# Optimization experiments

Hardware: AMD Instinct MI355X
Metric: run time of the kernel (lower is better)

The kernel has to match this reference:

```python
import jax, jax.numpy as jnp
import numpy as np

V, E, H2, B, T, OUT = 50000, 300, 512, 32, 512, 256
H = H2 // 2  # hidden per direction


def _rand_mask(key, lengths, n_true):
    # exactly n_true True positions per row, all within the valid prefix [0, len)
    t = jnp.arange(T)[None, :]
    r = jax.random.uniform(key, (B, T)) + (t >= lengths[:, None]) * 10.0
    idx = jnp.argsort(r, axis=1)[:, :n_true]
    mask = jnp.zeros((B, T), dtype=bool)
    return mask.at[jnp.arange(B)[:, None], idx].set(True)


def setup_inputs() -> dict:
    key = jax.random.key(0)
    ks = jax.random.split(key, 12)
    inputs = jax.random.randint(ks[0], (B, T), 0, V)
    lengths = jnp.sort(jax.random.randint(ks[1], (B,), OUT, T + 1))[::-1]
    lengths = lengths.at[0].set(T)  # max length == padded length
    fmask = _rand_mask(ks[2], lengths, OUT)
    bmask = _rand_mask(ks[3], lengths, OUT)
    emb_scale = np.sqrt(3.0 / E).astype(np.float32)
    emb = jax.random.uniform(ks[4], (V, E), minval=-emb_scale, maxval=emb_scale, dtype=jnp.float32)
    k = 1.0 / np.sqrt(H).astype(np.float32)
    def u(kk, shape):
        return jax.random.uniform(kk, shape, minval=-k, maxval=k, dtype=jnp.float32)
    return {
        'inputs': inputs, 'seq_length': lengths, 'fmask': fmask, 'bmask': bmask,
        'out_seq_length': OUT, 'emb': emb,
        'W_ih_f': u(ks[5], (4 * H, E)), 'W_hh_f': u(ks[6], (4 * H, H)),
        'b_ih_f': u(ks[7], (4 * H,)), 'b_hh_f': u(ks[8], (4 * H,)),
        'W_ih_b': u(ks[9], (4 * H, E)), 'W_hh_b': u(ks[10], (4 * H, H)),
        'b_ih_b': u(ks[11], (4 * H,)), 'b_hh_b': u(ks[7], (4 * H,)),
    }


def run_lstm(xe, W_ih, W_hh, b_ih, b_hh):
    # PyTorch LSTM cell, gate order i,f,g,o. xe: (B,T,E) -> (B,T,H)
    xg = jnp.einsum('bte,ge->btg', xe, W_ih) + (b_ih + b_hh)
    def step(carry, xg_t):
        h, c = carry
        g = xg_t + h @ W_hh.T
        i, f, gg, o = jnp.split(g, 4, axis=-1)
        c = jax.nn.sigmoid(f) * c + jax.nn.sigmoid(i) * jnp.tanh(gg)
        h = jax.nn.sigmoid(o) * jnp.tanh(c)
        return (h, c), h
    h0 = jnp.zeros((xe.shape[0], W_hh.shape[1]), xe.dtype)
    _, hs = jax.lax.scan(step, (h0, h0), xg.transpose(1, 0, 2))
    return hs.transpose(1, 0, 2)


def select_masked(x, mask, out_len):
    # masked_select row-major order == indices of True in increasing t
    idx = jnp.argsort(jnp.logical_not(mask), axis=1, stable=True)[:, :out_len]
    return jnp.take_along_axis(x, idx[:, :, None], axis=1)


def reference(inputs, seq_length, fmask, bmask, out_seq_length, emb,
              W_ih_f, W_hh_f, b_ih_f, b_hh_f, W_ih_b, W_hh_b, b_ih_b, b_hh_b):
    t = jnp.arange(inputs.shape[1])[None, :]          # (1,T)
    valid = t < seq_length[:, None]                   # (B,T)
    # forward direction (dropout is identity at inference)
    f_out = run_lstm(emb[inputs], W_ih_f, W_hh_f, b_ih_f, b_hh_f)
    f_out = f_out * valid[..., None]                  # pad_packed zeros beyond len
    fsel = select_masked(f_out, fmask, out_seq_length)
    # per-batch sequence reversal of valid prefix (padding stays in place)
    rev_idx = jnp.where(valid, seq_length[:, None] - 1 - t, t)
    rinputs = jnp.take_along_axis(inputs, rev_idx, axis=1)
    b_out = run_lstm(emb[rinputs], W_ih_b, W_hh_b, b_ih_b, b_hh_b)
    b_out = b_out * valid[..., None]
    bsel = select_masked(b_out, bmask, out_seq_length)
    # re-reverse selected backward outputs per batch
    k = jnp.minimum(seq_length, out_seq_length)[:, None]
    t2 = jnp.arange(out_seq_length)[None, :]
    idx2 = jnp.where(t2 < k, out_seq_length - 1 - t2, t2 - k)
    bsel = jnp.take_along_axis(bsel, idx2[:, :, None], axis=1)
    return jnp.concatenate([fsel, bsel], axis=2)      # (B,out_seq,2H)
```

## Files before the change

### kernel.cpp

```cpp
#include <hip/hip_runtime.h>
#include <hip/hip_bf16.h>

#define B_   32
#define T_   512
#define E_   300
#define H_   256
#define OUT_ 256
#define ECH  100
#define GROWP 293

typedef unsigned long long u64;

__global__ __launch_bounds__(64) void slots_kernel(
    const unsigned char* __restrict__ fm, const unsigned char* __restrict__ bm,
    int* __restrict__ fslot, int* __restrict__ bpos)
{
    __shared__ unsigned char fL[B_ * T_];
    __shared__ unsigned char bL[B_ * T_];
    const int tid = threadIdx.x;

    const unsigned int* fw = (const unsigned int*)fm;
    int cnt = 0;
    for (int i = tid; i < 128; i += 64) {
        unsigned int v = fw[i];
        cnt += ((v & 0xFFu) != 0) + ((v & 0xFF00u) != 0)
             + ((v & 0xFF0000u) != 0) + ((v >> 24) != 0);
    }
#pragma unroll
    for (int off = 32; off; off >>= 1) cnt += __shfl_down(cnt, off, 64);
    bool isbool = __shfl(cnt, 0, 64) > 128;

    if (isbool) {
        for (int i = tid; i < B_ * T_ / 4; i += 64) {
            ((unsigned int*)fL)[i] = ((const unsigned int*)fm)[i];
            ((unsigned int*)bL)[i] = ((const unsigned int*)bm)[i];
        }
    } else {
        const unsigned int* bw = (const unsigned int*)bm;
        for (int i = tid; i < B_ * T_; i += 64) {
            fL[i] = fw[i] != 0;
            bL[i] = bw[i] != 0;
        }
    }
    __syncthreads();

    if (tid < B_) {
        int jf = 0, jb = 0;
        for (int t = 0; t < T_; ++t) {
            bool f = fL[tid * T_ + t] != 0;
            bool g = bL[tid * T_ + t] != 0;
            fslot[tid * T_ + t] = f ? (jf++) : -1;
            bpos [tid * T_ + t] = g ? (OUT_ - 1 - (jb++)) : -1;
        }
    }
}

__global__ __launch_bounds__(256) void xg_gemm(
    const int* __restrict__ inputs, const int* __restrict__ seqlen,
    const float* __restrict__ emb,
    const float* __restrict__ Wihf, const float* __restrict__ Wihb,
    const float* __restrict__ bihf, const float* __restrict__ bhhf,
    const float* __restrict__ bihb, const float* __restrict__ bhhb,
    float* __restrict__ xg, int t0, int TcMax)
{
    const int tg   = blockIdx.y;
    const int dir  = blockIdx.z;
    const int rblk = blockIdx.x * 64;
    const int tid  = threadIdx.x;

    __shared__ float eL[4][B_][ECH];
    __shared__ int   tokS[4][B_];

    if (tid < 128) {
        int t4 = tid >> 5, b = tid & 31;
        int t = t0 + tg * 4 + t4;
        int L = seqlen[b];
        int tt = t;
        if (dir) tt = (t < L) ? (L - 1 - t) : t;
        tokS[t4][b] = inputs[b * T_ + tt];
    }

    const float* W = dir ? Wihb : Wihf;
    const int b  = tid & 31;
    const int r8 = tid >> 5;

    float acc[4][8];
#pragma unroll
    for (int t4 = 0; t4 < 4; ++t4)
#pragma unroll
        for (int m = 0; m < 8; ++m) acc[t4][m] = 0.f;

    for (int ec = 0; ec < 3; ++ec) {
        __syncthreads();
        for (int idx = tid; idx < 3200; idx += 256) {
            int q  = idx % 25;
            int bb = (idx / 25) & 31;
            int t4 = idx / (25 * 32);
            const float* erow = emb + (size_t)tokS[t4][bb] * E_ + ec * ECH;
            *(float4*)&eL[t4][bb][q * 4] = *(const float4*)(erow + q * 4);
        }
        __syncthreads();

        for (int e4 = 0; e4 < 25; ++e4) {
            float4 w4[8];
#pragma unroll
            for (int m = 0; m < 8; ++m)
                w4[m] = *(const float4*)(W + (size_t)(rblk + r8 + m * 8) * E_
                                         + ec * ECH + e4 * 4);
#pragma unroll
            for (int t4 = 0; t4 < 4; ++t4) {
                float4 h4 = *(const float4*)&eL[t4][b][e4 * 4];
#pragma unroll
                for (int m = 0; m < 8; ++m)
                    acc[t4][m] += h4.x * w4[m].x + h4.y * w4[m].y
                                + h4.z * w4[m].z + h4.w * w4[m].w;
            }
        }
    }

    const float* bi = dir ? bihb : bihf;
    const float* bh = dir ? bhhb : bhhf;
#pragma unroll
    for (int t4 = 0; t4 < 4; ++t4) {
        float* outp = xg + (size_t)(dir * TcMax + tg * 4 + t4) * (1024 * B_);
#pragma unroll
        for (int m = 0; m < 8; ++m) {
            int row = rblk + r8 + m * 8;
            outp[(size_t)row * B_ + b] = acc[t4][m] + bi[row] + bh[row];
        }
    }
}

__global__ __launch_bounds__(512, 2) void fused_lstm(
    const int* __restrict__ inputs, const int* __restrict__ seqlen,
    const float* __restrict__ emb,
    const float* __restrict__ Wihf, const float* __restrict__ Whhf,
    const float* __restrict__ bihf, const float* __restrict__ bhhf,
    const float* __restrict__ Wihb, const float* __restrict__ Whhb,
    const float* __restrict__ bihb, const float* __restrict__ bhhb,
    const int* __restrict__ fslot, const int* __restrict__ bpos,
    float* __restrict__ hbuf, float* __restrict__ cbuf,
    int* __restrict__ barr, int* __restrict__ xgcnt,
    float* __restrict__ xg, float* __restrict__ out,
    int t0, int Tc, int fused)
{
    const int wg  = blockIdx.x;
    const int tid = threadIdx.x;
    __shared__ __align__(16) float smem[13824];

    if (wg >= 128) {
        float* eL   = smem;
        int*   tokS = (int*)(smem + 12800);
        const int hw = wg - 128;

        for (int j = hw; j < 2048; j += 128) {
            const int tg  = j >> 4;
            const int dir = (j >> 3) & 1;
            const int rp  = j & 7;
            const int rblk = (rp * 2 + (tid >> 8)) * 64;

            if (tid < 128) {
                int t4 = tid >> 5, b = tid & 31;
                int t = tg * 4 + t4;
                int L = seqlen[b];
                int tt = t;
                if (dir) tt = (t < L) ? (L - 1 - t) : t;
                tokS[t4 * B_ + b] = inputs[b * T_ + tt];
            }

            const float* W  = dir ? Wihb : Wihf;
            const int ltid = tid & 255;
            const int b  = ltid & 31;
            const int r8 = ltid >> 5;

            float acc[4][8];
#pragma unroll
            for (int t4 = 0; t4 < 4; ++t4)
#pragma unroll
                for (int m = 0; m < 8; ++m) acc[t4][m] = 0.f;

            for (int ec = 0; ec < 3; ++ec) {
                __syncthreads();
                for (int idx = tid; idx < 3200; idx += 512) {
                    int q  = idx % 25;
                    int bb = (idx / 25) & 31;
                    int t4 = idx / (25 * 32);
                    const float* erow = emb + (size_t)tokS[t4 * B_ + bb] * E_ + ec * ECH;
                    *(float4*)&eL[(t4 * B_ + bb) * ECH + q * 4] = *(const float4*)(erow + q * 4);
                }
                __syncthreads();

                for (int e4 = 0; e4 < 25; ++e4) {
                    float4 w4[8];
#pragma unroll
                    for (int m = 0; m < 8; ++m)
                        w4[m] = *(const float4*)(W + (size_t)(rblk + r8 + m * 8) * E_
                                                 + ec * ECH + e4 * 4);
#pragma unroll
                    for (int t4 = 0; t4 < 4; ++t4) {
                        float4 h4 = *(const float4*)&eL[(t4 * B_ + b) * ECH + e4 * 4];
#pragma unroll
                        for (int m = 0; m < 8; ++m)
                            acc[t4][m] += h4.x * w4[m].x + h4.y * w4[m].y
                                        + h4.z * w4[m].z + h4.w * w4[m].w;
                    }
                }
            }

            const float* bi = dir ? bihb : bihf;
            const float* bh = dir ? bhhb : bhhf;
#pragma unroll
            for (int t4 = 0; t4 < 4; ++t4) {
                float* outp = xg + (size_t)(dir * 512 + tg * 4 + t4) * (1024 * B_);
#pragma unroll
                for (int m = 0; m < 8; ++m) {
                    int row = rblk + r8 + m * 8;
                    __hip_atomic_store(&outp[(size_t)row * B_ + b],
                                       acc[t4][m] + bi[row] + bh[row],
                                       __ATOMIC_RELAXED, __HIP_MEMORY_SCOPE_AGENT);
                }
            }
            __syncthreads();
            if (tid == 0)
                __hip_atomic_fetch_add(&xgcnt[dir * 128 + tg], 1,
                                       __ATOMIC_RELAXED, __HIP_MEMORY_SCOPE_AGENT);
        }
        return;
    }

    float* hP   = smem;
    float* gbuf = smem + 8704;
    int*   sL   = (int*)(smem + 8704 + 4688);

    const int dir = wg >> 6;
    const int wgd = wg & 63;
    const int u0  = wgd * 4;

    const int rg  = tid & 3;
    const int bgr = (tid >> 2) & 7;
    const int kq  = tid >> 5;
    const int wv  = tid >> 6;
    const int lane = tid & 63;

    const float* Whh = dir ? Whhb : Whhf;

    float w[4][16];
#pragma unroll
    for (int r = 0; r < 4; ++r) {
        const float* wr = Whh + (size_t)(rg * H_ + u0 + r) * H_ + kq * 16;
#pragma unroll
        for (int q = 0; q < 4; ++q) {
            float4 v = *(const float4*)(wr + q * 4);
            w[r][q * 4 + 0] = v.x; w[r][q * 4 + 1] = v.y;
            w[r][q * 4 + 2] = v.z; w[r][q * 4 + 3] = v.w;
        }
    }
    if (tid < B_) sL[tid] = seqlen[tid];
    __syncthreads();

    const int ul = (tid >> 5) & 3, bb = tid & 31;
    float c_reg = 0.f;
    if (t0 > 0 && tid < 128)
        c_reg = cbuf[(size_t)(dir * 64 + wgd) * 128 + ul * 32 + bb];

    if (fused) {
        if (tid == 0) {
            const int* xc = xgcnt + dir * 128 + (t0 >> 2);
            while (__hip_atomic_load(xc, __ATOMIC_RELAXED,
                                     __HIP_MEMORY_SCOPE_AGENT) < 8)
                __builtin_amdgcn_s_sleep(1);
        }
        __syncthreads();
    }
    float xgv0 = 0.f, xgv1 = 0.f, xgv2 = 0.f, xgv3 = 0.f;
    if (tid < 128) {
        const float* xp = xg + (size_t)(dir * Tc) * 32768 + (u0 + ul) * 32 + bb;
        xgv0 = __hip_atomic_load(xp, __ATOMIC_RELAXED, __HIP_MEMORY_SCOPE_AGENT);
        xgv1 = __hip_atomic_load(xp + 256 * 32, __ATOMIC_RELAXED, __HIP_MEMORY_SCOPE_AGENT);
        xgv2 = __hip_atomic_load(xp + 512 * 32, __ATOMIC_RELAXED, __HIP_MEMORY_SCOPE_AGENT);
        xgv3 = __hip_atomic_load(xp + 768 * 32, __ATOMIC_RELAXED, __HIP_MEMORY_SCOPE_AGENT);
    }

    int* myflag = barr + dir * 64 + wgd;

    for (int tc = 0; tc < Tc; ++tc) {
        const int t = t0 + tc;

        if (tc > 0) {
            const int* fp = barr + dir * 64 + wv + 8 * (lane & 7);
            const int gneed = (fused && wv < 2 && tc + 1 < Tc) ? ((t0 + tc + 1) >> 2) : -1;
            const int* xc = xgcnt + dir * 128 + (gneed < 0 ? 0 : gneed);
            for (;;) {
                bool ok = __hip_atomic_load(fp, __ATOMIC_RELAXED,
                                            __HIP_MEMORY_SCOPE_AGENT) >= tc;
                if (gneed >= 0)
                    ok = ok && (__hip_atomic_load(xc, __ATOMIC_RELAXED,
                                                  __HIP_MEMORY_SCOPE_AGENT) >= 8);
                if (__all(ok)) break;
                __builtin_amdgcn_s_sleep(1);
            }
        }

        float xgn0 = 0.f, xgn1 = 0.f, xgn2 = 0.f, xgn3 = 0.f;
        if (tc + 1 < Tc && tid < 128) {
            const float* xp = xg + (size_t)(dir * Tc + tc + 1) * 32768 + (u0 + ul) * 32 + bb;
            xgn0 = __hip_atomic_load(xp, __ATOMIC_RELAXED, __HIP_MEMORY_SCOPE_AGENT);
            xgn1 = __hip_atomic_load(xp + 256 * 32, __ATOMIC_RELAXED, __HIP_MEMORY_SCOPE_AGENT);
            xgn2 = __hip_atomic_load(xp + 512 * 32, __ATOMIC_RELAXED, __HIP_MEMORY_SCOPE_AGENT);
            xgn3 = __hip_atomic_load(xp + 768 * 32, __ATOMIC_RELAXED, __HIP_MEMORY_SCOPE_AGENT);
        }

        if (t > 0) {
            const u64* hp64 = (const u64*)(hbuf +
                (size_t)(dir * 2 + ((t - 1) & 1)) * 8192);
            u64 hr[8];
#pragma unroll
            for (int i = 0; i < 8; ++i)
                hr[i] = __hip_atomic_load(hp64 + tid + 512 * i, __ATOMIC_RELAXED,
                                          __HIP_MEMORY_SCOPE_AGENT);
#pragma unroll
            for (int i = 0; i < 8; ++i) {
                int j = tid + 512 * i;
                int k  = (j >> 6) * 4 + ((j >> 4) & 3);
                int b0 = (j & 15) * 2;
                int addr = ((k >> 4) * 8 + (b0 >> 2)) * 68 + (k & 15) * 4 + (b0 & 3);
                *(u64*)&hP[addr] = hr[i];
            }
        }
        __syncthreads();

        float acc[4][4];
#pragma unroll
        for (int r = 0; r < 4; ++r)
#pragma unroll
            for (int bi = 0; bi < 4; ++bi) acc[r][bi] = 0.f;

        if (t > 0) {
            const float* hblk = &hP[(kq * 8 + bgr) * 68];
#pragma unroll
            for (int kk = 0; kk < 16; ++kk) {
                float4 h4 = *(const float4*)(hblk + kk * 4);
#pragma unroll
                for (int r = 0; r < 4; ++r) {
                    acc[r][0] += w[r][kk] * h4.x;
                    acc[r][1] += w[r][kk] * h4.y;
                    acc[r][2] += w[r][kk] * h4.z;
                    acc[r][3] += w[r][kk] * h4.w;
                }
            }
        }

#pragma unroll
        for (int r = 0; r < 4; ++r)
#pragma unroll
            for (int bi = 0; bi < 4; ++bi)
                acc[r][bi] += __shfl_xor(acc[r][bi], 32, 64);

        if (((tid >> 5) & 1) == 0) {
            const int kq2 = kq >> 1;
#pragma unroll
            for (int r = 0; r < 4; ++r)
#pragma unroll
                for (int bi = 0; bi < 4; ++bi)
                    gbuf[(r * 4 + rg) * GROWP + (bgr * 4 + bi) * 9 + kq2] = acc[r][bi];
        }
        __syncthreads();

        float hnew = 0.f;
        float* oaddr = nullptr;
        if (tid < 128) {
            const int u = u0 + ul;
            if (t < sL[bb]) {
                float gi = xgv0, gf = xgv1, gg = xgv2, go = xgv3;
#pragma unroll
                for (int q = 0; q < 8; ++q) {
                    gi += gbuf[(ul * 4 + 0) * GROWP + bb * 9 + q];
                    gf += gbuf[(ul * 4 + 1) * GROWP + bb * 9 + q];
                    gg += gbuf[(ul * 4 + 2) * GROWP + bb * 9 + q];
                    go += gbuf[(ul * 4 + 3) * GROWP + bb * 9 + q];
                }
                float si = 1.f / (1.f + expf(-gi));
                float sf = 1.f / (1.f + expf(-gf));
                float so = 1.f / (1.f + expf(-go));
                c_reg = sf * c_reg + si * tanhf(gg);
                hnew  = so * tanhf(c_reg);
                if (dir == 0) {
                    int j = fslot[bb * T_ + t];
                    if (j >= 0) oaddr = &out[((size_t)bb * OUT_ + j) * 512 + u];
                } else {
                    int p = bpos[bb * T_ + t];
                    if (p >= 0) oaddr = &out[((size_t)bb * OUT_ + p) * 512 + 256 + u];
                }
            } else {
                hnew = hP[((u >> 4) * 8 + (bb >> 2)) * 68 + (u & 15) * 4 + (bb & 3)];
            }
            float* hn = hbuf + (size_t)(dir * 2 + (t & 1)) * 8192;
            __hip_atomic_store(&hn[wgd * 128 + tid], hnew,
                               __ATOMIC_RELAXED, __HIP_MEMORY_SCOPE_AGENT);
        }
        xgv0 = xgn0; xgv1 = xgn1; xgv2 = xgn2; xgv3 = xgn3;
        __syncthreads();

        if (tc + 1 < Tc && tid == 0)
            __hip_atomic_store(myflag, tc + 1, __ATOMIC_RELAXED,
                               __HIP_MEMORY_SCOPE_AGENT);
        if (oaddr)
            __hip_atomic_store(oaddr, hnew, __ATOMIC_RELAXED,
                               __HIP_MEMORY_SCOPE_AGENT);
    }

    if (tid < 128)
        cbuf[(size_t)(dir * 64 + wgd) * 128 + ul * 32 + bb] = c_reg;
}

extern "C" void kernel_launch(void* const* d_in, const int* in_sizes, int n_in,
                              void* d_out, int out_size, void* d_ws, size_t ws_size,
                              hipStream_t stream) {
    const int*           inputs = (const int*)d_in[0];
    const int*           seqlen = (const int*)d_in[1];
    const unsigned char* fm     = (const unsigned char*)d_in[2];
    const unsigned char* bm     = (const unsigned char*)d_in[3];
    const float* emb  = (const float*)d_in[5];
    const float* Wihf = (const float*)d_in[6];
    const float* Whhf = (const float*)d_in[7];
    const float* bihf = (const float*)d_in[8];
    const float* bhhf = (const float*)d_in[9];
    const float* Wihb = (const float*)d_in[10];
    const float* Whhb = (const float*)d_in[11];
    const float* bihb = (const float*)d_in[12];
    const float* bhhb = (const float*)d_in[13];
    float* out = (float*)d_out;

    char* ws = (char*)d_ws;
    int*   fslot = (int*)(ws);
    int*   bpos  = (int*)(ws + 65536);
    float* hbuf  = (float*)(ws + 131072);
    float* cbuf  = (float*)(ws + 262144);
    int*   barr  = (int*)(ws + 327680);
    int*   xgcnt = (int*)(ws + 328192);
    float* xg    = (float*)(ws + 393216);
    (void)in_sizes; (void)n_in; (void)out_size;

    size_t avail = (ws_size > 393216) ? ws_size - 393216 : 0;
    int Tc = 4;
    for (int c = 512; c >= 4; c >>= 1)
        if ((size_t)c * 262144 <= avail) { Tc = c; break; }

    slots_kernel<<<1, 64, 0, stream>>>(fm, bm, fslot, bpos);

    if (Tc == 512) {
        (void)hipMemsetAsync(barr, 0, 512 + 1024, stream);
        fused_lstm<<<256, 512, 0, stream>>>(
            inputs, seqlen, emb, Wihf, Whhf, bihf, bhhf,
            Wihb, Whhb, bihb, bhhb, fslot, bpos,
            hbuf, cbuf, barr, xgcnt, xg, out, 0, 512, 1);
    } else {
        for (int t0 = 0; t0 < T_; t0 += Tc) {
            dim3 g(16, Tc / 4, 2);
            xg_gemm<<<g, 256, 0, stream>>>(inputs, seqlen, emb, Wihf, Wihb,
                                           bihf, bhhf, bihb, bhhb, xg, t0, Tc);
            (void)hipMemsetAsync(barr, 0, 512 + 1024, stream);
            fused_lstm<<<128, 512, 0, stream>>>(
                inputs, seqlen, emb, Wihf, Whhf, bihf, bhhf,
                Wihb, Whhb, bihb, bhhb, fslot, bpos,
                hbuf, cbuf, barr, xgcnt, xg, out, t0, Tc, 0);
        }
    }
}
```

Measured before the change: 2.039 ms.

## Replace flag barrier with step-tagged hidden-state packets and deepen xg prefetch

Each hidden value is now written as a 64-bit packet that carries the timestep alongside the float, so consumer workgroups spin directly on the h data instead of polling per-workgroup flags and then loading h separately. This removes one round trip through global memory and the separate flag store from every recurrent step. The input-gate prefetch now runs two steps ahead, and the wait on the xg producer counter moves off the critical path. In exchange the h traffic doubles in size, each poll reads 16 u64 values per thread, and hbuf must be zeroed up front.

```diff
diff --git a/kernel.cpp b/kernel.cpp
--- a/kernel.cpp
+++ b/kernel.cpp
@@ -139,9 +139,8 @@
     const float* __restrict__ Wihb, const float* __restrict__ Whhb,
     const float* __restrict__ bihb, const float* __restrict__ bhhb,
     const int* __restrict__ fslot, const int* __restrict__ bpos,
-    float* __restrict__ hbuf, float* __restrict__ cbuf,
-    int* __restrict__ barr, int* __restrict__ xgcnt,
-    float* __restrict__ xg, float* __restrict__ out,
+    u64* __restrict__ hbuf, float* __restrict__ cbuf,
+    int* __restrict__ xgcnt, float* __restrict__ xg, float* __restrict__ out,
     int t0, int Tc, int fused)
 {
     const int wg  = blockIdx.x;
@@ -239,8 +238,6 @@
     const int rg  = tid & 3;
     const int bgr = (tid >> 2) & 7;
     const int kq  = tid >> 5;
-    const int wv  = tid >> 6;
-    const int lane = tid & 63;
 
     const float* Whh = dir ? Whhb : Whhf;
 
@@ -272,62 +269,56 @@
         }
         __syncthreads();
     }
-    float xgv0 = 0.f, xgv1 = 0.f, xgv2 = 0.f, xgv3 = 0.f;
+    float xv0 = 0.f, xv1 = 0.f, xv2 = 0.f, xv3 = 0.f;
+    float ya0 = 0.f, ya1 = 0.f, ya2 = 0.f, ya3 = 0.f;
     if (tid < 128) {
         const float* xp = xg + (size_t)(dir * Tc) * 32768 + (u0 + ul) * 32 + bb;
-        xgv0 = __hip_atomic_load(xp, __ATOMIC_RELAXED, __HIP_MEMORY_SCOPE_AGENT);
-        xgv1 = __hip_atomic_load(xp + 256 * 32, __ATOMIC_RELAXED, __HIP_MEMORY_SCOPE_AGENT);
-        xgv2 = __hip_atomic_load(xp + 512 * 32, __ATOMIC_RELAXED, __HIP_MEMORY_SCOPE_AGENT);
-        xgv3 = __hip_atomic_load(xp + 768 * 32, __ATOMIC_RELAXED, __HIP_MEMORY_SCOPE_AGENT);
-    }
-
-    int* myflag = barr + dir * 64 + wgd;
+        xv0 = __hip_atomic_load(xp,         __ATOMIC_RELAXED, __HIP_MEMORY_SCOPE_AGENT);
+        xv1 = __hip_atomic_load(xp +  8192, __ATOMIC_RELAXED, __HIP_MEMORY_SCOPE_AGENT);
+        xv2 = __hip_atomic_load(xp + 16384, __ATOMIC_RELAXED, __HIP_MEMORY_SCOPE_AGENT);
+        xv3 = __hip_atomic_load(xp + 24576, __ATOMIC_RELAXED, __HIP_MEMORY_SCOPE_AGENT);
+        if (Tc > 1) {
+            const float* xq = xp + 32768;
+            ya0 = __hip_atomic_load(xq,         __ATOMIC_RELAXED, __HIP_MEMORY_SCOPE_AGENT);
+            ya1 = __hip_atomic_load(xq +  8192, __ATOMIC_RELAXED, __HIP_MEMORY_SCOPE_AGENT);
+            ya2 = __hip_atomic_load(xq + 16384, __ATOMIC_RELAXED, __HIP_MEMORY_SCOPE_AGENT);
+            ya3 = __hip_atomic_load(xq + 24576, __ATOMIC_RELAXED, __HIP_MEMORY_SCOPE_AGENT);
+        }
+    }
 
     for (int tc = 0; tc < Tc; ++tc) {
         const int t = t0 + tc;
 
-        if (tc > 0) {
-            const int* fp = barr + dir * 64 + wv + 8 * (lane & 7);
-            const int gneed = (fused && wv < 2 && tc + 1 < Tc) ? ((t0 + tc + 1) >> 2) : -1;
-            const int* xc = xgcnt + dir * 128 + (gneed < 0 ? 0 : gneed);
+        if (t > 0) {
+            const u64* hp = hbuf + (size_t)(dir * 2 + ((t - 1) & 1)) * 8192;
+            u64 hr[16];
             for (;;) {
-                bool ok = __hip_atomic_load(fp, __ATOMIC_RELAXED,
-                                            __HIP_MEMORY_SCOPE_AGENT) >= tc;
-                if (gneed >= 0)
-                    ok = ok && (__hip_atomic_load(xc, __ATOMIC_RELAXED,
-                                                  __HIP_MEMORY_SCOPE_AGENT) >= 8);
+#pragma unroll
+                for (int i = 0; i < 16; ++i)
+                    hr[i] = __hip_atomic_load(hp + tid + 512 * i, __ATOMIC_RELAXED,
+                                              __HIP_MEMORY_SCOPE_AGENT);
+                bool ok = true;
+#pragma unroll
+                for (int i = 0; i < 16; ++i)
+                    ok &= ((unsigned)(hr[i] >> 32) == (unsigned)t);
                 if (__all(ok)) break;
                 __builtin_amdgcn_s_sleep(1);
             }
-        }
-
-        float xgn0 = 0.f, xgn1 = 0.f, xgn2 = 0.f, xgn3 = 0.f;
-        if (tc + 1 < Tc && tid < 128) {
-            const float* xp = xg + (size_t)(dir * Tc + tc + 1) * 32768 + (u0 + ul) * 32 + bb;
-            xgn0 = __hip_atomic_load(xp, __ATOMIC_RELAXED, __HIP_MEMORY_SCOPE_AGENT);
-            xgn1 = __hip_atomic_load(xp + 256 * 32, __ATOMIC_RELAXED, __HIP_MEMORY_SCOPE_AGENT);
-            xgn2 = __hip_atomic_load(xp + 512 * 32, __ATOMIC_RELAXED, __HIP_MEMORY_SCOPE_AGENT);
-            xgn3 = __hip_atomic_load(xp + 768 * 32, __ATOMIC_RELAXED, __HIP_MEMORY_SCOPE_AGENT);
-        }
-
-        if (t > 0) {
-            const u64* hp64 = (const u64*)(hbuf +
-                (size_t)(dir * 2 + ((t - 1) & 1)) * 8192);
-            u64 hr[8];
-#pragma unroll
-            for (int i = 0; i < 8; ++i)
-                hr[i] = __hip_atomic_load(hp64 + tid + 512 * i, __ATOMIC_RELAXED,
-                                          __HIP_MEMORY_SCOPE_AGENT);
-#pragma unroll
-            for (int i = 0; i < 8; ++i) {
-                int j = tid + 512 * i;
-                int k  = (j >> 6) * 4 + ((j >> 4) & 3);
-                int b0 = (j & 15) * 2;
-                int addr = ((k >> 4) * 8 + (b0 >> 2)) * 68 + (k & 15) * 4 + (b0 & 3);
-                *(u64*)&hP[addr] = hr[i];
-            }
-        }
-        __syncthreads();
+#pragma unroll
+            for (int i = 0; i < 16; ++i) {
+                int wdx = tid + 512 * i;
+                int k = ((wdx >> 7) << 2) | ((wdx >> 5) & 3);
+                int b = wdx & 31;
+                hP[((k >> 4) * 8 + (b >> 2)) * 68 + (k & 15) * 4 + (b & 3)] =
+                    __uint_as_float((unsigned)hr[i]);
+            }
+        }
+        __syncthreads();
+
+        int cnt = 8;
+        if (fused && tc + 2 < Tc && tid < 128)
+            cnt = __hip_atomic_load(xgcnt + dir * 128 + ((t0 + tc + 2) >> 2),
+                                    __ATOMIC_RELAXED, __HIP_MEMORY_SCOPE_AGENT);
 
         float acc[4][4];
 #pragma unroll
@@ -371,7 +362,7 @@
         if (tid < 128) {
             const int u = u0 + ul;
             if (t < sL[bb]) {
-                float gi = xgv0, gf = xgv1, gg = xgv2, go = xgv3;
+                float gi = xv0, gf = xv1, gg = xv2, go = xv3;
 #pragma unroll
                 for (int q = 0; q < 8; ++q) {
                     gi += gbuf[(ul * 4 + 0) * GROWP + bb * 9 + q];
@@ -394,19 +385,32 @@
             } else {
                 hnew = hP[((u >> 4) * 8 + (bb >> 2)) * 68 + (u & 15) * 4 + (bb & 3)];
             }
-            float* hn = hbuf + (size_t)(dir * 2 + (t & 1)) * 8192;
-            __hip_atomic_store(&hn[wgd * 128 + tid], hnew,
+            u64 pkt = ((u64)(unsigned)(t + 1) << 32) | (u64)__float_as_uint(hnew);
+            u64* hn = hbuf + (size_t)(dir * 2 + (t & 1)) * 8192;
+            __hip_atomic_store(&hn[wgd * 128 + tid], pkt,
                                __ATOMIC_RELAXED, __HIP_MEMORY_SCOPE_AGENT);
         }
-        xgv0 = xgn0; xgv1 = xgn1; xgv2 = xgn2; xgv3 = xgn3;
-        __syncthreads();
-
-        if (tc + 1 < Tc && tid == 0)
-            __hip_atomic_store(myflag, tc + 1, __ATOMIC_RELAXED,
-                               __HIP_MEMORY_SCOPE_AGENT);
+        __syncthreads();
+
+        float z0 = 0.f, z1 = 0.f, z2 = 0.f, z3 = 0.f;
+        if (tc + 2 < Tc && tid < 128) {
+            if (fused && cnt < 8) {
+                const int* xc = xgcnt + dir * 128 + ((t0 + tc + 2) >> 2);
+                while (__hip_atomic_load(xc, __ATOMIC_RELAXED,
+                                         __HIP_MEMORY_SCOPE_AGENT) < 8)
+                    __builtin_amdgcn_s_sleep(1);
+            }
+            const float* xp = xg + (size_t)(dir * Tc + tc + 2) * 32768 + (u0 + ul) * 32 + bb;
+            z0 = __hip_atomic_load(xp,         __ATOMIC_RELAXED, __HIP_MEMORY_SCOPE_AGENT);
+            z1 = __hip_atomic_load(xp +  8192, __ATOMIC_RELAXED, __HIP_MEMORY_SCOPE_AGENT);
+            z2 = __hip_atomic_load(xp + 16384, __ATOMIC_RELAXED, __HIP_MEMORY_SCOPE_AGENT);
+            z3 = __hip_atomic_load(xp + 24576, __ATOMIC_RELAXED, __HIP_MEMORY_SCOPE_AGENT);
+        }
         if (oaddr)
             __hip_atomic_store(oaddr, hnew, __ATOMIC_RELAXED,
                                __HIP_MEMORY_SCOPE_AGENT);
+        xv0 = ya0; xv1 = ya1; xv2 = ya2; xv3 = ya3;
+        ya0 = z0;  ya1 = z1;  ya2 = z2;  ya3 = z3;
     }
 
     if (tid < 128)
@@ -434,36 +438,35 @@
     char* ws = (char*)d_ws;
     int*   fslot = (int*)(ws);
     int*   bpos  = (int*)(ws + 65536);
-    float* hbuf  = (float*)(ws + 131072);
-    float* cbuf  = (float*)(ws + 262144);
-    int*   barr  = (int*)(ws + 327680);
-    int*   xgcnt = (int*)(ws + 328192);
-    float* xg    = (float*)(ws + 393216);
+    u64*   hbuf  = (u64*)(ws + 131072);
+    float* cbuf  = (float*)(ws + 393216);
+    int*   xgcnt = (int*)(ws + 458752);
+    float* xg    = (float*)(ws + 460800);
     (void)in_sizes; (void)n_in; (void)out_size;
 
-    size_t avail = (ws_size > 393216) ? ws_size - 393216 : 0;
+    size_t avail = (ws_size > 460800) ? ws_size - 460800 : 0;
     int Tc = 4;
     for (int c = 512; c >= 4; c >>= 1)
         if ((size_t)c * 262144 <= avail) { Tc = c; break; }
 
+    (void)hipMemsetAsync(ws + 131072, 0, 262144, stream);
+    (void)hipMemsetAsync(ws + 458752, 0, 1024, stream);
     slots_kernel<<<1, 64, 0, stream>>>(fm, bm, fslot, bpos);
 
     if (Tc == 512) {
-        (void)hipMemsetAsync(barr, 0, 512 + 1024, stream);
         fused_lstm<<<256, 512, 0, stream>>>(
             inputs, seqlen, emb, Wihf, Whhf, bihf, bhhf,
             Wihb, Whhb, bihb, bhhb, fslot, bpos,
-            hbuf, cbuf, barr, xgcnt, xg, out, 0, 512, 1);
+            hbuf, cbuf, xgcnt, xg, out, 0, 512, 1);
     } else {
         for (int t0 = 0; t0 < T_; t0 += Tc) {
             dim3 g(16, Tc / 4, 2);
             xg_gemm<<<g, 256, 0, stream>>>(inputs, seqlen, emb, Wihf, Wihb,
                                            bihf, bhhf, bihb, bhhb, xg, t0, Tc);
-            (void)hipMemsetAsync(barr, 0, 512 + 1024, stream);
             fused_lstm<<<128, 512, 0, stream>>>(
                 inputs, seqlen, emb, Wihf, Whhf, bihf, bhhf,
                 Wihb, Whhb, bihb, bhhb, fslot, bpos,
-                hbuf, cbuf, barr, xgcnt, xg, out, t0, Tc, 0);
+                hbuf, cbuf, xgcnt, xg, out, t0, Tc, 0);
         }
     }
 }
```

Result: faster. 1.998 ms (median of 2 runs) (-2.0%).
